# Optimization experiments

Hardware: AMD Instinct MI355X
Metric: run time of the kernel (lower is better)

The kernel has to match this reference:

```python
import jax, jax.numpy as jnp
import numpy as np

B, S, H = 2, 2048, 3072
NQ, NKV, HD = 24, 8, 128
ROT = 96  # floor(128 * 0.75)
BASE = 10000.0


def _rope(x, rotary_dim, base=BASE, start_index=0):
    # x: [b, s, h, rotary_dim]; keras_hub GPT-NeoX style half-rotation
    s = x.shape[1]
    inv_freq = 1.0 / (base ** (jnp.arange(0, rotary_dim, 2, dtype=jnp.float32) / rotary_dim))
    pos = jnp.arange(s, dtype=jnp.float32) + start_index
    freq = pos[:, None] * inv_freq[None, :]            # [s, rot/2]
    emb = jnp.concatenate([freq, freq], axis=-1)       # [s, rot]
    cos = jnp.cos(emb)[None, :, None, :]
    sin = jnp.sin(emb)[None, :, None, :]
    x1, x2 = jnp.split(x, 2, axis=-1)
    half_rot = jnp.concatenate([-x2, x1], axis=-1)
    return x * cos + half_rot * sin


def setup_inputs() -> dict:
    key = jax.random.key(0)
    k1, k2, k3, k4, k5 = jax.random.split(key, 5)
    hidden_states = jax.random.normal(k1, (B, S, H), dtype=jnp.float32)
    # causal mask [B, S, S]
    attention_mask = jnp.broadcast_to(jnp.tril(jnp.ones((S, S), dtype=bool)), (B, S, S))
    scale = 0.02
    Wq = jax.random.normal(k2, (H, NQ, HD), dtype=jnp.float32) * scale
    Wk = jax.random.normal(k3, (H, NKV, HD), dtype=jnp.float32) * scale
    Wv = jax.random.normal(k4, (H, NKV, HD), dtype=jnp.float32) * scale
    Wo = jax.random.normal(k5, (NQ, HD, H), dtype=jnp.float32) * scale
    return {"hidden_states": hidden_states, "attention_mask": attention_mask,
            "Wq": Wq, "Wk": Wk, "Wv": Wv, "Wo": Wo}


def reference(hidden_states, attention_mask, Wq, Wk, Wv, Wo):
    groups = NQ // NKV
    inv_norm = 1.0 / np.sqrt(HD)
    q = jnp.einsum('bqm,muh->bquh', hidden_states, Wq)   # [B,S,NQ,HD]
    k = jnp.einsum('bkm,mvh->bkvh', hidden_states, Wk)   # [B,S,NKV,HD]
    v = jnp.einsum('bkm,mvh->bkvh', hidden_states, Wv)
    # partial RoPE on first ROT dims
    q = jnp.concatenate([_rope(q[..., :ROT], ROT), q[..., ROT:]], axis=-1)
    k = jnp.concatenate([_rope(k[..., :ROT], ROT), k[..., ROT:]], axis=-1)
    # GQA: repeat kv heads (interleaved, matches ops.repeat axis=2)
    k = jnp.repeat(k, groups, axis=2)
    v = jnp.repeat(v, groups, axis=2)
    scores = jnp.einsum('bquh,bkuh->buqk', q, k) * inv_norm  # [B,NQ,S,S]
    scores = scores.astype(jnp.float32)
    scores = jnp.where(attention_mask[:, None, :, :], scores, -1e9)
    probs = jax.nn.softmax(scores, axis=-1).astype(hidden_states.dtype)
    attn = jnp.einsum('buqk,bkuh->bquh', probs, v)           # [B,S,NQ,HD]
    return jnp.einsum('bquh,uhm->bqm', attn, Wo)             # [B,S,H]
```

## Files before the change

### kernel.cpp

```cpp
#include <hip/hip_runtime.h>
#include <hip/hip_bf16.h>
#include <cstdint>

namespace {

constexpr int Bn = 2, Sn = 2048, Hn = 3072, NQn = 24, NKVn = 8, HDn = 128;
constexpr int LDQKV = NQn * HDn + 2 * NKVn * HDn;
constexpr int KCOLo = NQn * HDn;
constexpr int VCOLo = KCOLo + NKVn * HDn;

typedef __attribute__((ext_vector_type(8))) __bf16 bf16x8;
typedef __attribute__((ext_vector_type(4))) float f32x4;
typedef __attribute__((ext_vector_type(8))) unsigned short u16x8;
typedef __attribute__((ext_vector_type(4))) unsigned short u16x4;

__device__ __forceinline__ unsigned short f2bf(float f) {
  union { float f; unsigned u; } v; v.f = f;
  return (unsigned short)((v.u + 0x7fffu + ((v.u >> 16) & 1u)) >> 16);
}
__device__ __forceinline__ float bf2f(unsigned short u) {
  union { unsigned u; float f; } v; v.u = ((unsigned)u) << 16;
  return v.f;
}
__device__ __forceinline__ void gload_lds16(const void* g, void* l) {
  __builtin_amdgcn_global_load_lds(
      (__attribute__((address_space(1))) void*)(uintptr_t)g,
      (__attribute__((address_space(3))) void*)(uintptr_t)l, 16, 0, 0);
}

__global__ void build_rope_tab(float* __restrict__ cosT, float* __restrict__ sinT) {
  int idx = blockIdx.x * 256 + threadIdx.x;
  if (idx >= Sn * 48) return;
  int s = idx / 48, i = idx % 48;
  float invf = exp2f(-(float)i * (13.287712379549449f / 48.f));
  float f = (float)s * invf;
  cosT[idx] = cosf(f);
  sinT[idx] = sinf(f);
}

__global__ void cvt_f32_bf16(const float* __restrict__ in, unsigned short* __restrict__ out, int n) {
  int i = (blockIdx.x * 256 + threadIdx.x) * 4;
  int stride = gridDim.x * 256 * 4;
  for (; i < n; i += stride) {
    float4 v = *(const float4*)&in[i];
    u16x4 o;
    o[0] = f2bf(v.x); o[1] = f2bf(v.y); o[2] = f2bf(v.z); o[3] = f2bf(v.w);
    *(u16x4*)&out[i] = o;
  }
}

__global__ void transpose_cvt(const float* __restrict__ in, unsigned short* __restrict__ out,
                              int K, int N) {
  __shared__ float tile[32][33];
  int bx = blockIdx.x * 32;
  int by = blockIdx.y * 32;
  int tx = threadIdx.x & 31, ty = threadIdx.x >> 5;
#pragma unroll
  for (int r = ty; r < 32; r += 8)
    tile[r][tx] = in[(size_t)(by + r) * N + bx + tx];
  __syncthreads();
#pragma unroll
  for (int r = ty; r < 32; r += 8)
    out[(size_t)(bx + r) * K + by + tx] = f2bf(tile[tx][r]);
}

template <int BF16OUT>
__launch_bounds__(256, 2)
__global__ void gemm_tn(const unsigned short* __restrict__ A, const unsigned short* __restrict__ Bm,
                        void* __restrict__ Cout, int M, int N, int K) {
  __shared__ unsigned short Atile[128 * 32];
  __shared__ unsigned short Btile[128 * 32];
  const int t = threadIdx.x;
  const int lane = t & 63, w = t >> 6;
  const int wr = w >> 1, wc = w & 1;
  const int brow = blockIdx.y * 128, bcol = blockIdx.x * 128;
  f32x4 acc[4][4] = {};
  const int nK = K >> 5;
  const int r0 = t >> 2, ko0 = (t & 3) * 8;
  const unsigned short* Ab = A + (size_t)brow * K;
  const unsigned short* Bb = Bm + (size_t)bcol * K;
  char* Al0 = (char*)Atile + w * 1024;
  char* Al1 = (char*)Atile + 4096 + w * 1024;
  char* Bl0 = (char*)Btile + w * 1024;
  char* Bl1 = (char*)Btile + 4096 + w * 1024;
  const int l15 = lane & 15, lk = (lane >> 4) * 8;

  for (int kt = 0; kt < nK; ++kt) {
    const int k0 = kt * 32;
    __syncthreads();
    gload_lds16(Ab + (size_t)r0 * K + k0 + ko0, Al0);
    gload_lds16(Ab + (size_t)(r0 + 64) * K + k0 + ko0, Al1);
    gload_lds16(Bb + (size_t)r0 * K + k0 + ko0, Bl0);
    gload_lds16(Bb + (size_t)(r0 + 64) * K + k0 + ko0, Bl1);
    __syncthreads();
    bf16x8 aF[4], bF[4];
#pragma unroll
    for (int m = 0; m < 4; ++m)
      aF[m] = *(const bf16x8*)&Atile[(wr * 64 + m * 16 + l15) * 32 + lk];
#pragma unroll
    for (int n = 0; n < 4; ++n)
      bF[n] = *(const bf16x8*)&Btile[(wc * 64 + n * 16 + l15) * 32 + lk];
#pragma unroll
    for (int m = 0; m < 4; ++m)
#pragma unroll
      for (int n = 0; n < 4; ++n)
        acc[m][n] = __builtin_amdgcn_mfma_f32_16x16x32_bf16(aF[m], bF[n], acc[m][n], 0, 0, 0);
  }
  const int lr = (lane >> 4) * 4, lc = lane & 15;
  if (BF16OUT) {
    unsigned short* C = (unsigned short*)Cout;
#pragma unroll
    for (int m = 0; m < 4; ++m) {
      int row = brow + wr * 64 + m * 16 + lr;
#pragma unroll
      for (int n = 0; n < 4; ++n) {
        int col = bcol + wc * 64 + n * 16 + lc;
#pragma unroll
        for (int i = 0; i < 4; ++i)
          C[(size_t)(row + i) * N + col] = f2bf(acc[m][n][i]);
      }
    }
  } else {
    float* C = (float*)Cout;
#pragma unroll
    for (int m = 0; m < 4; ++m) {
      int row = brow + wr * 64 + m * 16 + lr;
#pragma unroll
      for (int n = 0; n < 4; ++n) {
        int col = bcol + wc * 64 + n * 16 + lc;
#pragma unroll
        for (int i = 0; i < 4; ++i)
          C[(size_t)(row + i) * N + col] = acc[m][n][i];
      }
    }
  }
}

__global__ void rope_kernel(unsigned short* __restrict__ QKV, const float* __restrict__ cosT,
                            const float* __restrict__ sinT) {
  int rid = blockIdx.x;
  int s = rid & (Sn - 1);
  unsigned short* row = QKV + (size_t)rid * LDQKV;
  for (int p = threadIdx.x; p < 32 * 48; p += 256) {
    int h = p / 48, i = p % 48;
    int col = (h < NQn) ? h * HDn : KCOLo + (h - NQn) * HDn;
    float c = cosT[s * 48 + i], sn = sinT[s * 48 + i];
    float x1 = bf2f(row[col + i]), x2 = bf2f(row[col + i + 48]);
    row[col + i] = f2bf(x1 * c - x2 * sn);
    row[col + i + 48] = f2bf(x2 * c + x1 * sn);
  }
}

__launch_bounds__(256, 2)
__global__ void attn_kernel(const unsigned short* __restrict__ QKV, unsigned short* __restrict__ O) {
  __shared__ unsigned short Klds[64 * 128];
  __shared__ unsigned short Vlds[128 * 64];
  __shared__ unsigned short Plds[4][16 * 64];
  const int t = threadIdx.x, lane = t & 63, w = t >> 6;
  const int bq = blockIdx.x;
  const int hid = blockIdx.y;
  const int b = hid / NQn, u = hid % NQn, kv = u / 3;
  const int l15 = lane & 15, lh = lane >> 4;

  bf16x8 qf[4];
  {
    int qrow = bq * 64 + w * 16 + l15;
    const unsigned short* qp = QKV + (size_t)(b * Sn + qrow) * LDQKV + u * HDn;
#pragma unroll
    for (int f = 0; f < 4; ++f) qf[f] = *(const bf16x8*)(qp + f * 32 + lh * 8);
  }
  float mrow[4], lrow[4];
  f32x4 Oa[8] = {};
#pragma unroll
  for (int i = 0; i < 4; ++i) { mrow[i] = -1e30f; lrow[i] = 0.f; }
  const float cscale = 0.08838834764831845f * 1.4426950408889634f;

  const unsigned short* Kg = QKV + (size_t)(b * Sn) * LDQKV + KCOLo + kv * HDn;
  const unsigned short* Vg = QKV + (size_t)(b * Sn) * LDQKV + VCOLo + kv * HDn;

  for (int kt = 0; kt <= bq; ++kt) {
    __syncthreads();
#pragma unroll
    for (int iter = 0; iter < 4; ++iter) {
      int c = iter * 256 + t;
      int krow = c >> 4, pch = c & 15;
      int hch = (pch & 8) | ((pch & 7) ^ (krow & 7));
      gload_lds16(Kg + (size_t)(kt * 64 + krow) * LDQKV + hch * 8,
                  (char*)Klds + (iter * 256 + w * 64) * 16);
    }
    u16x8 vtmp[4];
#pragma unroll
    for (int iter = 0; iter < 4; ++iter) {
      int c = iter * 256 + t;
      vtmp[iter] = *(const u16x8*)(Vg + (size_t)(kt * 64 + (c >> 4)) * LDQKV + (c & 15) * 8);
    }
#pragma unroll
    for (int iter = 0; iter < 4; ++iter) {
      int c = iter * 256 + t;
      int r = c >> 4, hd0 = (c & 15) * 8;
#pragma unroll
      for (int j = 0; j < 8; ++j) {
        int hd = hd0 + j;
        int f = (hd & 7) ^ ((hd >> 3) & 7);
        int pos = ((r >> 3) ^ f) & 7;
        Vlds[hd * 64 + pos * 8 + (r & 7)] = vtmp[iter][j];
      }
    }
    __syncthreads();
    f32x4 Sg[4] = {};
#pragma unroll
    for (int g = 0; g < 4; ++g) {
      int kcol = g * 16 + l15;
#pragma unroll
      for (int s = 0; s < 4; ++s) {
        int h = s * 4 + lh;
        int p = (h & 8) | ((h & 7) ^ (kcol & 7));
        bf16x8 kf = *(const bf16x8*)&Klds[kcol * 128 + p * 8];
        Sg[g] = __builtin_amdgcn_mfma_f32_16x16x32_bf16(qf[s], kf, Sg[g], 0, 0, 0);
      }
    }
    float P[4][4];
    const bool last = (kt == bq);
#pragma unroll
    for (int g = 0; g < 4; ++g)
#pragma unroll
      for (int i = 0; i < 4; ++i) {
        float sv = Sg[g][i] * cscale;
        if (last) {
          int colw = g * 16 + l15;
          int roww = w * 16 + lh * 4 + i;
          if (colw > roww) sv = -1e30f;
        }
        P[g][i] = sv;
      }
    float rs[4];
#pragma unroll
    for (int i = 0; i < 4; ++i) {
      float pm = fmaxf(fmaxf(P[0][i], P[1][i]), fmaxf(P[2][i], P[3][i]));
#pragma unroll
      for (int msk = 1; msk < 16; msk <<= 1) pm = fmaxf(pm, __shfl_xor(pm, msk, 64));
      float mn = fmaxf(mrow[i], pm);
      rs[i] = exp2f(mrow[i] - mn);
      mrow[i] = mn;
      float ps = 0.f;
#pragma unroll
      for (int g = 0; g < 4; ++g) { float e = exp2f(P[g][i] - mn); P[g][i] = e; ps += e; }
#pragma unroll
      for (int msk = 1; msk < 16; msk <<= 1) ps += __shfl_xor(ps, msk, 64);
      lrow[i] = lrow[i] * rs[i] + ps;
    }
#pragma unroll
    for (int g = 0; g < 8; ++g)
#pragma unroll
      for (int i = 0; i < 4; ++i) Oa[g][i] *= rs[i];
    unsigned short* pl = Plds[w];
#pragma unroll
    for (int g = 0; g < 4; ++g) {
      int k = g * 16 + l15, ch = k >> 3;
#pragma unroll
      for (int i = 0; i < 4; ++i) {
        int q = lh * 4 + i;
        int pos = (ch ^ (q & 7)) & 7;
        pl[q * 64 + pos * 8 + (k & 7)] = f2bf(P[g][i]);
      }
    }
#pragma unroll
    for (int kk = 0; kk < 2; ++kk) {
      int ch = kk * 4 + lh;
      int posp = (ch ^ (l15 & 7)) & 7;
      bf16x8 pf = *(const bf16x8*)&pl[l15 * 64 + posp * 8];
#pragma unroll
      for (int g = 0; g < 8; ++g) {
        int hd = g * 16 + l15;
        int f = (hd & 7) ^ ((hd >> 3) & 7);
        int vpos = (ch ^ f) & 7;
        bf16x8 vf = *(const bf16x8*)&Vlds[hd * 64 + vpos * 8];
        Oa[g] = __builtin_amdgcn_mfma_f32_16x16x32_bf16(pf, vf, Oa[g], 0, 0, 0);
      }
    }
  }
#pragma unroll
  for (int i = 0; i < 4; ++i) {
    float inv = 1.0f / lrow[i];
    int qrow = bq * 64 + w * 16 + lh * 4 + i;
    unsigned short* op = O + (size_t)(b * Sn + qrow) * (NQn * HDn) + u * HDn;
#pragma unroll
    for (int g = 0; g < 8; ++g) op[g * 16 + l15] = f2bf(Oa[g][i] * inv);
  }
}

}

extern "C" void kernel_launch(void* const* d_in, const int* in_sizes, int n_in,
                              void* d_out, int out_size, void* d_ws, size_t ws_size,
                              hipStream_t stream) {
  const float* hidden = (const float*)d_in[0];
  const float* Wq = (const float*)d_in[2];
  const float* Wk = (const float*)d_in[3];
  const float* Wv = (const float*)d_in[4];
  const float* Wo = (const float*)d_in[5];
  float* out = (float*)d_out;

  char* ws = (char*)d_ws;
  constexpr size_t szXb = (size_t)Bn * Sn * Hn * 2;
  constexpr size_t szWqkv = (size_t)LDQKV * Hn * 2;
  constexpr size_t szQKV = (size_t)Bn * Sn * LDQKV * 2;
  constexpr size_t szTab = (size_t)Sn * 48 * 4;
  constexpr size_t szTotal = szXb + szWqkv + szQKV + 2 * szTab;
  if (ws_size < szTotal) return;

  unsigned short* Xb = (unsigned short*)(ws);
  unsigned short* Obuf = Xb;
  unsigned short* Wqkv = (unsigned short*)(ws + szXb);
  unsigned short* Wob = Wqkv;
  unsigned short* QKV = (unsigned short*)(ws + szXb + szWqkv);
  float* cosT = (float*)(ws + szXb + szWqkv + szQKV);
  float* sinT = (float*)(ws + szXb + szWqkv + szQKV + szTab);

  build_rope_tab<<<(Sn * 48 + 255) / 256, 256, 0, stream>>>(cosT, sinT);
  cvt_f32_bf16<<<3072, 256, 0, stream>>>(hidden, Xb, Bn * Sn * Hn);
  transpose_cvt<<<dim3(96, 96), 256, 0, stream>>>(Wq, Wqkv, Hn, NQn * HDn);
  transpose_cvt<<<dim3(32, 96), 256, 0, stream>>>(Wk, Wqkv + (size_t)KCOLo * Hn, Hn, NKVn * HDn);
  transpose_cvt<<<dim3(32, 96), 256, 0, stream>>>(Wv, Wqkv + (size_t)VCOLo * Hn, Hn, NKVn * HDn);
  gemm_tn<1><<<dim3(LDQKV / 128, (Bn * Sn) / 128), 256, 0, stream>>>(Xb, Wqkv, QKV,
                                                                    Bn * Sn, LDQKV, Hn);
  transpose_cvt<<<dim3(96, 96), 256, 0, stream>>>(Wo, Wob, Hn, Hn);
  rope_kernel<<<Bn * Sn, 256, 0, stream>>>(QKV, cosT, sinT);
  attn_kernel<<<dim3(Sn / 64, Bn * NQn), 256, 0, stream>>>(QKV, Obuf);
  gemm_tn<0><<<dim3(Hn / 128, (Bn * Sn) / 128), 256, 0, stream>>>(Obuf, Wob, out,
                                                                  Bn * Sn, Hn, Hn);
}
```

Before: 779.0 us.

## Pre-transpose V and double-buffer K/V tiles with async LDS loads in attention

```diff
diff --git a/kernel.cpp b/kernel.cpp
--- a/kernel.cpp
+++ b/kernel.cpp
@@ -11,7 +11,6 @@
 
 typedef __attribute__((ext_vector_type(8))) __bf16 bf16x8;
 typedef __attribute__((ext_vector_type(4))) float f32x4;
-typedef __attribute__((ext_vector_type(8))) unsigned short u16x8;
 typedef __attribute__((ext_vector_type(4))) unsigned short u16x4;
 
 __device__ __forceinline__ unsigned short f2bf(float f) {
@@ -62,6 +61,21 @@
 #pragma unroll
   for (int r = ty; r < 32; r += 8)
     out[(size_t)(bx + r) * K + by + tx] = f2bf(tile[tx][r]);
+}
+
+__global__ void transpose_v(const unsigned short* __restrict__ QKV, unsigned short* __restrict__ VT) {
+  __shared__ unsigned short tile[32][33];
+  int s0 = blockIdx.x * 32;
+  int b = blockIdx.y >> 5;
+  int vc0 = (blockIdx.y & 31) * 32;
+  int tx = threadIdx.x & 31, ty = threadIdx.x >> 5;
+#pragma unroll
+  for (int r = ty; r < 32; r += 8)
+    tile[r][tx] = QKV[(size_t)(b * Sn + s0 + r) * LDQKV + VCOLo + vc0 + tx];
+  __syncthreads();
+#pragma unroll
+  for (int r = ty; r < 32; r += 8)
+    VT[(size_t)(b * (NKVn * HDn) + vc0 + r) * Sn + s0 + tx] = tile[tx][r];
 }
 
 template <int BF16OUT>
@@ -152,12 +166,14 @@
 }
 
 __launch_bounds__(256, 2)
-__global__ void attn_kernel(const unsigned short* __restrict__ QKV, unsigned short* __restrict__ O) {
-  __shared__ unsigned short Klds[64 * 128];
-  __shared__ unsigned short Vlds[128 * 64];
+__global__ void attn_kernel(const unsigned short* __restrict__ QKV,
+                            const unsigned short* __restrict__ VT,
+                            unsigned short* __restrict__ O) {
+  __shared__ unsigned short Klds[2][64 * 128];
+  __shared__ unsigned short Vlds[2][128 * 64];
   __shared__ unsigned short Plds[4][16 * 64];
   const int t = threadIdx.x, lane = t & 63, w = t >> 6;
-  const int bq = blockIdx.x;
+  const int bq = gridDim.x - 1 - blockIdx.x;
   const int hid = blockIdx.y;
   const int b = hid / NQn, u = hid % NQn, kv = u / 3;
   const int l15 = lane & 15, lh = lane >> 4;
@@ -176,38 +192,41 @@
   const float cscale = 0.08838834764831845f * 1.4426950408889634f;
 
   const unsigned short* Kg = QKV + (size_t)(b * Sn) * LDQKV + KCOLo + kv * HDn;
-  const unsigned short* Vg = QKV + (size_t)(b * Sn) * LDQKV + VCOLo + kv * HDn;
-
-  for (int kt = 0; kt <= bq; ++kt) {
-    __syncthreads();
+  const unsigned short* Vg = VT + (size_t)(b * NKVn + kv) * HDn * Sn;
+
+  auto stageK = [&](int kt, int buf) {
 #pragma unroll
     for (int iter = 0; iter < 4; ++iter) {
       int c = iter * 256 + t;
       int krow = c >> 4, pch = c & 15;
       int hch = (pch & 8) | ((pch & 7) ^ (krow & 7));
       gload_lds16(Kg + (size_t)(kt * 64 + krow) * LDQKV + hch * 8,
-                  (char*)Klds + (iter * 256 + w * 64) * 16);
-    }
-    u16x8 vtmp[4];
+                  (char*)&Klds[buf][0] + (iter * 256 + w * 64) * 16);
+    }
+  };
+  auto stageV = [&](int kt, int buf) {
 #pragma unroll
     for (int iter = 0; iter < 4; ++iter) {
       int c = iter * 256 + t;
-      vtmp[iter] = *(const u16x8*)(Vg + (size_t)(kt * 64 + (c >> 4)) * LDQKV + (c & 15) * 8);
-    }
-#pragma unroll
-    for (int iter = 0; iter < 4; ++iter) {
-      int c = iter * 256 + t;
-      int r = c >> 4, hd0 = (c & 15) * 8;
-#pragma unroll
-      for (int j = 0; j < 8; ++j) {
-        int hd = hd0 + j;
-        int f = (hd & 7) ^ ((hd >> 3) & 7);
-        int pos = ((r >> 3) ^ f) & 7;
-        Vlds[hd * 64 + pos * 8 + (r & 7)] = vtmp[iter][j];
-      }
-    }
-    __syncthreads();
+      int hd = c >> 3, p = c & 7;
+      int sch = p ^ (hd & 7);
+      gload_lds16(Vg + (size_t)hd * Sn + kt * 64 + sch * 8,
+                  (char*)&Vlds[buf][0] + (iter * 256 + w * 64) * 16);
+    }
+  };
+
+  const int nt = bq + 1;
+  stageK(0, 0);
+  stageV(0, 0);
+  __syncthreads();
+
+  for (int kt = 0; kt < nt; ++kt) {
+    const int cur = kt & 1;
+    if (kt + 1 < nt) { stageK(kt + 1, cur ^ 1); stageV(kt + 1, cur ^ 1); }
+    const unsigned short* Kb = &Klds[cur][0];
+    const unsigned short* Vb = &Vlds[cur][0];
     f32x4 Sg[4] = {};
+    __builtin_amdgcn_s_setprio(1);
 #pragma unroll
     for (int g = 0; g < 4; ++g) {
       int kcol = g * 16 + l15;
@@ -215,10 +234,11 @@
       for (int s = 0; s < 4; ++s) {
         int h = s * 4 + lh;
         int p = (h & 8) | ((h & 7) ^ (kcol & 7));
-        bf16x8 kf = *(const bf16x8*)&Klds[kcol * 128 + p * 8];
+        bf16x8 kf = *(const bf16x8*)&Kb[kcol * 128 + p * 8];
         Sg[g] = __builtin_amdgcn_mfma_f32_16x16x32_bf16(qf[s], kf, Sg[g], 0, 0, 0);
       }
     }
+    __builtin_amdgcn_s_setprio(0);
     float P[4][4];
     const bool last = (kt == bq);
 #pragma unroll
@@ -264,6 +284,7 @@
         pl[q * 64 + pos * 8 + (k & 7)] = f2bf(P[g][i]);
       }
     }
+    __builtin_amdgcn_s_setprio(1);
 #pragma unroll
     for (int kk = 0; kk < 2; ++kk) {
       int ch = kk * 4 + lh;
@@ -272,12 +293,13 @@
 #pragma unroll
       for (int g = 0; g < 8; ++g) {
         int hd = g * 16 + l15;
-        int f = (hd & 7) ^ ((hd >> 3) & 7);
-        int vpos = (ch ^ f) & 7;
-        bf16x8 vf = *(const bf16x8*)&Vlds[hd * 64 + vpos * 8];
+        int vpos = (ch ^ (hd & 7)) & 7;
+        bf16x8 vf = *(const bf16x8*)&Vb[hd * 64 + vpos * 8];
         Oa[g] = __builtin_amdgcn_mfma_f32_16x16x32_bf16(pf, vf, Oa[g], 0, 0, 0);
       }
     }
+    __builtin_amdgcn_s_setprio(0);
+    __syncthreads();
   }
 #pragma unroll
   for (int i = 0; i < 4; ++i) {
@@ -304,8 +326,11 @@
   char* ws = (char*)d_ws;
   constexpr size_t szXb = (size_t)Bn * Sn * Hn * 2;
   constexpr size_t szWqkv = (size_t)LDQKV * Hn * 2;
+  constexpr size_t szWo = (size_t)Hn * Hn * 2;
+  constexpr size_t szVT = (size_t)Bn * NKVn * HDn * Sn * 2;
   constexpr size_t szQKV = (size_t)Bn * Sn * LDQKV * 2;
   constexpr size_t szTab = (size_t)Sn * 48 * 4;
+  static_assert(szWo + szVT <= szWqkv, "Wob+VT must fit in Wqkv region");
   constexpr size_t szTotal = szXb + szWqkv + szQKV + 2 * szTab;
   if (ws_size < szTotal) return;
 
@@ -313,6 +338,7 @@
   unsigned short* Obuf = Xb;
   unsigned short* Wqkv = (unsigned short*)(ws + szXb);
   unsigned short* Wob = Wqkv;
+  unsigned short* VT = (unsigned short*)(ws + szXb + szWo);
   unsigned short* QKV = (unsigned short*)(ws + szXb + szWqkv);
   float* cosT = (float*)(ws + szXb + szWqkv + szQKV);
   float* sinT = (float*)(ws + szXb + szWqkv + szQKV + szTab);
@@ -325,8 +351,9 @@
   gemm_tn<1><<<dim3(LDQKV / 128, (Bn * Sn) / 128), 256, 0, stream>>>(Xb, Wqkv, QKV,
                                                                     Bn * Sn, LDQKV, Hn);
   transpose_cvt<<<dim3(96, 96), 256, 0, stream>>>(Wo, Wob, Hn, Hn);
+  transpose_v<<<dim3(Sn / 32, Bn * NKVn * HDn / 32), 256, 0, stream>>>(QKV, VT);
   rope_kernel<<<Bn * Sn, 256, 0, stream>>>(QKV, cosT, sinT);
-  attn_kernel<<<dim3(Sn / 64, Bn * NQn), 256, 0, stream>>>(QKV, Obuf);
+  attn_kernel<<<dim3(Sn / 64, Bn * NQn), 256, 0, stream>>>(QKV, VT, Obuf);
   gemm_tn<0><<<dim3(Hn / 128, (Bn * Sn) / 128), 256, 0, stream>>>(Obuf, Wob, out,
                                                                   Bn * Sn, Hn, Hn);
 }
```

Measured after the change: 733.0 us. 1.06x faster.
